# Kernel tuning notes

Measured on AMD Instinct MI355X. Metric: run time of the kernel, lower is better.

Reference implementation:

```python
import jax, jax.numpy as jnp
import numpy as np

SCALING = 32.0 / 16.0  # alpha / r

def setup_inputs() -> dict:
    key = jax.random.key(0)
    k1, k2, k3, k4 = jax.random.split(key, 4)
    B_, S, D_in, D_out, R = 4, 2048, 4096, 4096, 16
    x = jax.random.normal(k1, (B_, S, D_in), dtype=jnp.float32)
    W_base = jax.random.normal(k2, (D_out, D_in), dtype=jnp.float32) * 0.02
    b_base = jax.random.normal(k3, (D_out,), dtype=jnp.float32) * 0.02
    A = jax.random.normal(k4, (R, D_in), dtype=jnp.float32) * 0.02
    B = jnp.zeros((D_out, R), dtype=jnp.float32)  # lora_B init to zeros
    return {"x": x, "W_base": W_base, "b_base": b_base, "A": A, "B": B}

def reference(x, W_base, b_base, A, B):
    # base linear (stands in for dequantized 4-bit matmul): [B,S,Din] @ [Din,Dout]
    out = jnp.einsum('bsd,od->bso', x, W_base) + b_base
    # LoRA path: B(A(x)) * scaling, dropout=0 -> identity
    xa = jnp.einsum('bsd,rd->bsr', x, A)        # [B,S,r]
    delta = jnp.einsum('bsr,or->bso', xa, B)    # [B,S,Dout]
    return out + delta * SCALING
```

## Files before the change

### kernel.cpp

```cpp
#include <hip/hip_runtime.h>


typedef __attribute__((ext_vector_type(4)))  float f32x4;
typedef __attribute__((ext_vector_type(16))) float f32x16;
typedef __attribute__((ext_vector_type(8)))  short bf16x8;

__device__ __forceinline__ unsigned short f2bf(float f) {
    unsigned u = __builtin_bit_cast(unsigned, f);
    unsigned r = u + 0x7fffu + ((u >> 16) & 1u);
    return (unsigned short)(r >> 16);
}

__device__ __forceinline__ void gload_lds16(const void* g, void* l) {
    __builtin_amdgcn_global_load_lds(
        (const __attribute__((address_space(1))) void*)g,
        (__attribute__((address_space(3))) void*)l, 16, 0, 0);
}

__global__ __launch_bounds__(256) void cast_x_kernel(
    const float* __restrict__ x, unsigned short* __restrict__ xb, int n8)
{
    int stride = gridDim.x * blockDim.x;
    for (int i = blockIdx.x * blockDim.x + threadIdx.x; i < n8; i += stride) {
        size_t base = (size_t)i * 8;
        float4 f0 = *(const float4*)&x[base];
        float4 f1 = *(const float4*)&x[base + 4];
        ushort4 o0, o1;
        o0.x = f2bf(f0.x); o0.y = f2bf(f0.y); o0.z = f2bf(f0.z); o0.w = f2bf(f0.w);
        o1.x = f2bf(f1.x); o1.y = f2bf(f1.y); o1.z = f2bf(f1.z); o1.w = f2bf(f1.w);
        *(ushort4*)&xb[base]     = o0;
        *(ushort4*)&xb[base + 4] = o1;
    }
}

__global__ __launch_bounds__(256) void prep_w_kernel(
    const float* __restrict__ W, const float* __restrict__ A,
    const float* __restrict__ Bl, unsigned short* __restrict__ wb,
    int K, float scale)
{
    __shared__ float Bs[16][16];
    const int t = threadIdx.x;
    const int n0 = blockIdx.y * 16;
    const int k0 = blockIdx.x * 256;
    {
        int nl = t >> 4, r = t & 15;
        Bs[nl][r] = Bl[(size_t)(n0 + nl) * 16 + r];
    }
    __syncthreads();

    const int lane = t & 63;
    const int wv = t >> 6;
    const int k = k0 + lane * 4;

    float4 av[16];
#pragma unroll
    for (int r = 0; r < 16; ++r)
        av[r] = *(const float4*)&A[(size_t)r * K + k];

#pragma unroll
    for (int j = 0; j < 4; ++j) {
        const int nl = wv * 4 + j;
        const int n = n0 + nl;
        float4 w = *(const float4*)&W[(size_t)n * K + k];
        float d0 = 0.f, d1 = 0.f, d2 = 0.f, d3 = 0.f;
#pragma unroll
        for (int r = 0; r < 16; ++r) {
            float b = Bs[nl][r];
            d0 += b * av[r].x; d1 += b * av[r].y;
            d2 += b * av[r].z; d3 += b * av[r].w;
        }
        ushort4 o;
        o.x = f2bf(w.x + scale * d0);
        o.y = f2bf(w.y + scale * d1);
        o.z = f2bf(w.z + scale * d2);
        o.w = f2bf(w.w + scale * d3);
        *(ushort4*)&wb[(size_t)n * K + k] = o;
    }
}


#define SETPRIO(p) __builtin_amdgcn_s_setprio(p)
#define BARRIER()  __builtin_amdgcn_s_barrier()
#define LGKM0()    do { asm volatile("s_waitcnt lgkmcnt(0)" ::: "memory"); \
                        __builtin_amdgcn_sched_barrier(0); } while (0)

__global__ __launch_bounds__(512, 2) void gemm256_kernel(
    const unsigned short* __restrict__ Xb, const unsigned short* __restrict__ Wb,
    const float* __restrict__ bias, float* __restrict__ out,
    int M, int N, int K)
{
    __shared__ __align__(16) unsigned short lds[2][2][2][8192];

    const int NT = K / 64;
    const int ntn = N / 256;
    int bid = blockIdx.x;
    {
        int per = gridDim.x >> 3;
        bid = (bid & 7) * per + (bid >> 3);
    }
    const int tm = bid / ntn, tn = bid % ntn;

    const int t = threadIdx.x;
    const int lane = t & 63, wave = t >> 6;
    const int wr = wave >> 2;
    const int wc = wave & 3;
    const int wch = wc >> 1;
    const int bro = (wc & 1) * 64;

    const int srow = t >> 3;
    const int scol = ((t & 7) * 8) ^ (((t >> 3) & 7) << 3);
    unsigned gA[2][2], gB[2][2];
#pragma unroll
    for (int h = 0; h < 2; ++h)
#pragma unroll
        for (int i = 0; i < 2; ++i) {
            gA[h][i] = (unsigned)((tm * 256 + h * 128 + i * 64 + srow) * K + scol);
            gB[h][i] = (unsigned)((tn * 256 + h * 128 + i * 64 + srow) * K + scol);
        }

#define ST_A(buf, h, i, ktt)                                                    \
    gload_lds16(Xb + gA[h][i] + (ktt) * 64,                                     \
                &lds[buf][0][h][(i) * 4096 + wave * 512]);
#define ST_B(buf, h, i, ktt)                                                    \
    gload_lds16(Wb + gB[h][i] + (ktt) * 64,                                     \
                &lds[buf][1][h][(i) * 4096 + wave * 512]);

    const int r32 = lane & 31;
    const int hi2 = lane >> 5;
    const int bsw = (r32 & 7) << 4;
    int koff[4];
#pragma unroll
    for (int kq = 0; kq < 4; ++kq)
        koff[kq] = (kq * 32 + hi2 * 16) ^ bsw;

    f32x16 acc[4][2] = {};

#pragma unroll
    for (int h = 0; h < 2; ++h)
#pragma unroll
        for (int i = 0; i < 2; ++i) { ST_A(0, h, i, 0) ST_B(0, h, i, 0) }
#pragma unroll
    for (int h = 0; h < 2; ++h)
#pragma unroll
        for (int i = 0; i < 2; ++i) { ST_A(1, h, i, 1) }
    asm volatile("s_waitcnt vmcnt(4)" ::: "memory");
    BARRIER();

#define MFMA_PAIR(mb0, nb)                                                      \
    _Pragma("unroll") for (int kq = 0; kq < 4; ++kq) {                          \
        acc[mb0][nb] = __builtin_amdgcn_mfma_f32_32x32x16_bf16(                 \
            a[mb0][kq], b[nb][kq], acc[mb0][nb], 0, 0, 0);                      \
        acc[mb0 + 1][nb] = __builtin_amdgcn_mfma_f32_32x32x16_bf16(             \
            a[mb0 + 1][kq], b[nb][kq], acc[mb0 + 1][nb], 0, 0, 0);              \
    }

    for (int kt = 0; kt < NT; ++kt) {
        const int cur = kt & 1;
        const char* pA = (const char*)&lds[cur][0][wr][0];
        const char* pB = (const char*)&lds[cur][1][wch][0];
        const bool stB = (kt + 1 < NT);
        const bool stA = (kt + 2 < NT);

        bf16x8 a[4][4], b[2][4];

#pragma unroll
        for (int mb = 0; mb < 2; ++mb)
#pragma unroll
            for (int kq = 0; kq < 4; ++kq)
                a[mb][kq] = *(const bf16x8*)(pA + (mb * 32 + r32) * 128 + koff[kq]);
#pragma unroll
        for (int kq = 0; kq < 4; ++kq)
            b[0][kq] = *(const bf16x8*)(pB + (bro + r32) * 128 + koff[kq]);
        if (stB) { ST_B(cur ^ 1, 0, 0, kt + 1) ST_B(cur ^ 1, 0, 1, kt + 1) }
        BARRIER();
        LGKM0();
        SETPRIO(1);
        MFMA_PAIR(0, 0)
        SETPRIO(0);
        BARRIER();

#pragma unroll
        for (int mb = 2; mb < 4; ++mb)
#pragma unroll
            for (int kq = 0; kq < 4; ++kq)
                a[mb][kq] = *(const bf16x8*)(pA + (mb * 32 + r32) * 128 + koff[kq]);
        if (stB) { ST_B(cur ^ 1, 1, 0, kt + 1) ST_B(cur ^ 1, 1, 1, kt + 1) }
        BARRIER();
        LGKM0();
        SETPRIO(1);
        MFMA_PAIR(2, 0)
        SETPRIO(0);
        BARRIER();

#pragma unroll
        for (int kq = 0; kq < 4; ++kq)
            b[1][kq] = *(const bf16x8*)(pB + (bro + 32 + r32) * 128 + koff[kq]);
        if (stA) { ST_A(cur, 0, 0, kt + 2) ST_A(cur, 0, 1, kt + 2) }
        BARRIER();
        LGKM0();
        SETPRIO(1);
        MFMA_PAIR(0, 1)
        SETPRIO(0);
        BARRIER();

        if (stA) { ST_A(cur, 1, 0, kt + 2) ST_A(cur, 1, 1, kt + 2) }
        BARRIER();
        SETPRIO(1);
        MFMA_PAIR(2, 1)
        SETPRIO(0);
        if (stA) {
            asm volatile("s_waitcnt vmcnt(4)" ::: "memory");
        } else {
            asm volatile("s_waitcnt vmcnt(0)" ::: "memory");
        }
        BARRIER();
    }

    const int row0 = tm * 256 + wr * 128 + hi2 * 4;
    const int col0 = tn * 256 + wc * 64 + r32;
#pragma unroll
    for (int nb = 0; nb < 2; ++nb) {
        const int col = col0 + nb * 32;
        const float bv = bias[col];
#pragma unroll
        for (int mb = 0; mb < 4; ++mb) {
            const f32x16 v = acc[mb][nb];
#pragma unroll
            for (int r = 0; r < 16; ++r) {
                const int row = row0 + mb * 32 + (r & 3) + 8 * (r >> 2);
                out[(size_t)row * N + col] = v[r] + bv;
            }
        }
    }
}

extern "C" void kernel_launch(void* const* d_in, const int* in_sizes, int n_in,
                              void* d_out, int out_size, void* d_ws, size_t ws_size,
                              hipStream_t stream)
{
    const float* x  = (const float*)d_in[0];
    const float* W  = (const float*)d_in[1];
    const float* b  = (const float*)d_in[2];
    const float* A  = (const float*)d_in[3];
    const float* Bl = (const float*)d_in[4];
    float* out = (float*)d_out;

    const int Dout = in_sizes[2];
    const int Din  = in_sizes[1] / Dout;
    const int M    = in_sizes[0] / Din;

    unsigned short* xb = (unsigned short*)d_ws;
    unsigned short* wb = xb + (size_t)M * Din;

    cast_x_kernel<<<2048, 256, 0, stream>>>(x, xb, M * Din / 8);

    dim3 gw(Din / 256, Dout / 16);
    prep_w_kernel<<<gw, 256, 0, stream>>>(W, A, Bl, wb, Din, 2.0f);

    const int grid = (M / 256) * (Dout / 256);
    gemm256_kernel<<<grid, 512, 0, stream>>>(xb, wb, b, out, M, Dout, Din);
}
```

Baseline: 321.4 us.

## Use 4 waves per block with 128x128 per-wave tiles in GEMM

Cuts the GEMM block from 8 waves to 4 while keeping the 256x256 block tile, so each wave now computes a 128x128 sub-tile (16 accumulator tiles instead of 8). Each wave issues twice as many global-to-LDS loads, and the vmcnt waits are adjusted to match. The aim is more register-level reuse of A and B fragments and fewer LDS reads per MFMA. In exchange, accumulator register pressure doubles (256 VGPRs of accumulators), occupancy drops to one 4-wave block per launch-bounds setting, and there is less latency hiding.

```diff
diff --git a/kernel.cpp b/kernel.cpp
--- a/kernel.cpp
+++ b/kernel.cpp
@@ -84,7 +84,7 @@
 #define LGKM0()    do { asm volatile("s_waitcnt lgkmcnt(0)" ::: "memory"); \
                         __builtin_amdgcn_sched_barrier(0); } while (0)
 
-__global__ __launch_bounds__(512, 2) void gemm256_kernel(
+__global__ __launch_bounds__(256, 1) void gemm256_kernel(
     const unsigned short* __restrict__ Xb, const unsigned short* __restrict__ Wb,
     const float* __restrict__ bias, float* __restrict__ out,
     int M, int N, int K)
@@ -102,10 +102,8 @@
 
     const int t = threadIdx.x;
     const int lane = t & 63, wave = t >> 6;
-    const int wr = wave >> 2;
-    const int wc = wave & 3;
-    const int wch = wc >> 1;
-    const int bro = (wc & 1) * 64;
+    const int wr = wave >> 1;
+    const int wc = wave & 1;
 
     const int srow = t >> 3;
     const int scol = ((t & 7) * 8) ^ (((t >> 3) & 7) << 3);
@@ -117,13 +115,22 @@
             gA[h][i] = (unsigned)((tm * 256 + h * 128 + i * 64 + srow) * K + scol);
             gB[h][i] = (unsigned)((tn * 256 + h * 128 + i * 64 + srow) * K + scol);
         }
-
-#define ST_A(buf, h, i, ktt)                                                    \
-    gload_lds16(Xb + gA[h][i] + (ktt) * 64,                                     \
-                &lds[buf][0][h][(i) * 4096 + wave * 512]);
-#define ST_B(buf, h, i, ktt)                                                    \
-    gload_lds16(Wb + gB[h][i] + (ktt) * 64,                                     \
-                &lds[buf][1][h][(i) * 4096 + wave * 512]);
+    const unsigned jstep = 32u * (unsigned)K;
+
+#define ST_A(buf, h, ktt)                                                       \
+    _Pragma("unroll") for (int i = 0; i < 2; ++i) {                             \
+        gload_lds16(Xb + gA[h][i] + (ktt) * 64,                                 \
+                    &lds[buf][0][h][i * 4096 + wave * 512]);                    \
+        gload_lds16(Xb + gA[h][i] + jstep + (ktt) * 64,                         \
+                    &lds[buf][0][h][i * 4096 + 2048 + wave * 512]);             \
+    }
+#define ST_B(buf, h, ktt)                                                       \
+    _Pragma("unroll") for (int i = 0; i < 2; ++i) {                             \
+        gload_lds16(Wb + gB[h][i] + (ktt) * 64,                                 \
+                    &lds[buf][1][h][i * 4096 + wave * 512]);                    \
+        gload_lds16(Wb + gB[h][i] + jstep + (ktt) * 64,                         \
+                    &lds[buf][1][h][i * 4096 + 2048 + wave * 512]);             \
+    }
 
     const int r32 = lane & 31;
     const int hi2 = lane >> 5;
@@ -133,35 +140,32 @@
     for (int kq = 0; kq < 4; ++kq)
         koff[kq] = (kq * 32 + hi2 * 16) ^ bsw;
 
-    f32x16 acc[4][2] = {};
-
-#pragma unroll
-    for (int h = 0; h < 2; ++h)
-#pragma unroll
-        for (int i = 0; i < 2; ++i) { ST_A(0, h, i, 0) ST_B(0, h, i, 0) }
-#pragma unroll
-    for (int h = 0; h < 2; ++h)
-#pragma unroll
-        for (int i = 0; i < 2; ++i) { ST_A(1, h, i, 1) }
-    asm volatile("s_waitcnt vmcnt(4)" ::: "memory");
+    f32x16 acc[4][4] = {};
+
+#pragma unroll
+    for (int h = 0; h < 2; ++h) { ST_A(0, h, 0) ST_B(0, h, 0) }
+#pragma unroll
+    for (int h = 0; h < 2; ++h) { ST_A(1, h, 1) }
+    asm volatile("s_waitcnt vmcnt(8)" ::: "memory");
     BARRIER();
 
-#define MFMA_PAIR(mb0, nb)                                                      \
-    _Pragma("unroll") for (int kq = 0; kq < 4; ++kq) {                          \
-        acc[mb0][nb] = __builtin_amdgcn_mfma_f32_32x32x16_bf16(                 \
-            a[mb0][kq], b[nb][kq], acc[mb0][nb], 0, 0, 0);                      \
-        acc[mb0 + 1][nb] = __builtin_amdgcn_mfma_f32_32x32x16_bf16(             \
-            a[mb0 + 1][kq], b[nb][kq], acc[mb0 + 1][nb], 0, 0, 0);              \
-    }
+#define MFMA_QUAD(mbp, nbp)                                                     \
+    _Pragma("unroll") for (int kq = 0; kq < 4; ++kq)                            \
+    _Pragma("unroll") for (int d = 0; d < 2; ++d)                               \
+    _Pragma("unroll") for (int e = 0; e < 2; ++e)                               \
+        acc[2 * (mbp) + d][2 * (nbp) + e] =                                     \
+            __builtin_amdgcn_mfma_f32_32x32x16_bf16(                            \
+                a[2 * (mbp) + d][kq], b[2 * (nbp) + e][kq],                     \
+                acc[2 * (mbp) + d][2 * (nbp) + e], 0, 0, 0);
 
     for (int kt = 0; kt < NT; ++kt) {
         const int cur = kt & 1;
         const char* pA = (const char*)&lds[cur][0][wr][0];
-        const char* pB = (const char*)&lds[cur][1][wch][0];
+        const char* pB = (const char*)&lds[cur][1][wc][0];
         const bool stB = (kt + 1 < NT);
         const bool stA = (kt + 2 < NT);
 
-        bf16x8 a[4][4], b[2][4];
+        bf16x8 a[4][4], b[4][4];
 
 #pragma unroll
         for (int mb = 0; mb < 2; ++mb)
@@ -169,13 +173,15 @@
             for (int kq = 0; kq < 4; ++kq)
                 a[mb][kq] = *(const bf16x8*)(pA + (mb * 32 + r32) * 128 + koff[kq]);
 #pragma unroll
-        for (int kq = 0; kq < 4; ++kq)
-            b[0][kq] = *(const bf16x8*)(pB + (bro + r32) * 128 + koff[kq]);
-        if (stB) { ST_B(cur ^ 1, 0, 0, kt + 1) ST_B(cur ^ 1, 0, 1, kt + 1) }
+        for (int nb = 0; nb < 2; ++nb)
+#pragma unroll
+            for (int kq = 0; kq < 4; ++kq)
+                b[nb][kq] = *(const bf16x8*)(pB + (nb * 32 + r32) * 128 + koff[kq]);
+        if (stB) { ST_B(cur ^ 1, 0, kt + 1) }
         BARRIER();
         LGKM0();
         SETPRIO(1);
-        MFMA_PAIR(0, 0)
+        MFMA_QUAD(0, 0)
         SETPRIO(0);
         BARRIER();
 
@@ -184,32 +190,34 @@
 #pragma unroll
             for (int kq = 0; kq < 4; ++kq)
                 a[mb][kq] = *(const bf16x8*)(pA + (mb * 32 + r32) * 128 + koff[kq]);
-        if (stB) { ST_B(cur ^ 1, 1, 0, kt + 1) ST_B(cur ^ 1, 1, 1, kt + 1) }
+        if (stB) { ST_B(cur ^ 1, 1, kt + 1) }
         BARRIER();
         LGKM0();
         SETPRIO(1);
-        MFMA_PAIR(2, 0)
-        SETPRIO(0);
-        BARRIER();
-
-#pragma unroll
-        for (int kq = 0; kq < 4; ++kq)
-            b[1][kq] = *(const bf16x8*)(pB + (bro + 32 + r32) * 128 + koff[kq]);
-        if (stA) { ST_A(cur, 0, 0, kt + 2) ST_A(cur, 0, 1, kt + 2) }
+        MFMA_QUAD(1, 0)
+        SETPRIO(0);
+        BARRIER();
+
+#pragma unroll
+        for (int nb = 2; nb < 4; ++nb)
+#pragma unroll
+            for (int kq = 0; kq < 4; ++kq)
+                b[nb][kq] = *(const bf16x8*)(pB + (nb * 32 + r32) * 128 + koff[kq]);
+        if (stA) { ST_A(cur, 0, kt + 2) }
         BARRIER();
         LGKM0();
         SETPRIO(1);
-        MFMA_PAIR(0, 1)
-        SETPRIO(0);
-        BARRIER();
-
-        if (stA) { ST_A(cur, 1, 0, kt + 2) ST_A(cur, 1, 1, kt + 2) }
-        BARRIER();
-        SETPRIO(1);
-        MFMA_PAIR(2, 1)
+        MFMA_QUAD(0, 1)
+        SETPRIO(0);
+        BARRIER();
+
+        if (stA) { ST_A(cur, 1, kt + 2) }
+        BARRIER();
+        SETPRIO(1);
+        MFMA_QUAD(1, 1)
         SETPRIO(0);
         if (stA) {
-            asm volatile("s_waitcnt vmcnt(4)" ::: "memory");
+            asm volatile("s_waitcnt vmcnt(8)" ::: "memory");
         } else {
             asm volatile("s_waitcnt vmcnt(0)" ::: "memory");
         }
@@ -217,9 +225,9 @@
     }
 
     const int row0 = tm * 256 + wr * 128 + hi2 * 4;
-    const int col0 = tn * 256 + wc * 64 + r32;
-#pragma unroll
-    for (int nb = 0; nb < 2; ++nb) {
+    const int col0 = tn * 256 + wc * 128 + r32;
+#pragma unroll
+    for (int nb = 0; nb < 4; ++nb) {
         const int col = col0 + nb * 32;
         const float bv = bias[col];
 #pragma unroll
@@ -258,5 +266,5 @@
     prep_w_kernel<<<gw, 256, 0, stream>>>(W, A, Bl, wb, Din, 2.0f);
 
     const int grid = (M / 256) * (Dout / 256);
-    gemm256_kernel<<<grid, 512, 0, stream>>>(xb, wb, b, out, M, Dout, Din);
-}
+    gemm256_kernel<<<grid, 256, 0, stream>>>(xb, wb, b, out, M, Dout, Din);
+}
```

New measurement: 319.8 us. No clear change (-0.5%).
